# Optimization experiments

Hardware: AMD Instinct MI355X
Metric: run time of the kernel (lower is better)

The kernel has to match this reference:

```python
import jax, jax.numpy as jnp
import numpy as np

B, L, S = 4, 512, 100
NG, GS = 19, 5          # 19 clades of 5 species; species 95..99 are singleton clades
VOCAB = 6
HID = 512
HPOOL = 4               # num_attention_heads // 2
D = 64                  # hidden_size / num_attention_heads
ALL = HPOOL * D         # 256
FIRE_H = 32
TIME_SCALE = 1.0        # from time_enc = 'fire_1'
MAX_DIST = 20.0         # config.max_evol_dist


def setup_inputs() -> dict:
    key = jax.random.key(0)
    ks = jax.random.split(key, 10)
    return {
        "source_ids": jax.random.randint(ks[0], (B, L, S), 0, VOCAB, dtype=jnp.int32),
        "in_clade_phylo_dist": jax.random.uniform(ks[1], (S,), dtype=jnp.float32) * MAX_DIST,
        "attn_w_emb": jax.random.normal(ks[2], (VOCAB, HPOOL), dtype=jnp.float32) * 0.02,
        "value_emb": jax.random.normal(ks[3], (VOCAB, ALL), dtype=jnp.float32) * 0.02,
        "ffn_w": jax.random.normal(ks[4], (ALL, HID), dtype=jnp.float32) * 0.02,
        "ffn_b": jnp.zeros((HID,), dtype=jnp.float32),
        "embed_tab": jax.random.normal(ks[5], (VOCAB, HID), dtype=jnp.float32) * 0.02,
        "fire_c": jnp.float32(100.0),
        "fire_w1": jax.random.normal(ks[6], (FIRE_H,), dtype=jnp.float32) * 0.5,
        "fire_w2": jax.random.normal(ks[7], (FIRE_H,), dtype=jnp.float32) * 0.5,
    }


def reference(source_ids, in_clade_phylo_dist, attn_w_emb, value_emb,
              ffn_w, ffn_b, embed_tab, fire_c, fire_w1, fire_w2):
    # --- FIRE time bias: scalar MLP per species distance -> bias[s] ---
    c = jnp.maximum(fire_c, 0.0)
    rel = in_clade_phylo_dist * TIME_SCALE                      # [S]
    rel = jnp.log(c * rel + 1.0) / jnp.log(c * MAX_DIST + 1.0)  # [S]
    h = jax.nn.silu(rel[:, None] * fire_w1[None, :])            # [S, FIRE_H]
    bias = h @ fire_w2                                          # [S]

    # --- multi-species clades: embedding-based attention pooling ---
    grp = jnp.arange(NG * GS).reshape(NG, GS)                   # static clade layout
    ids_g = source_ids[..., :NG * GS].reshape(B, L, NG, GS)     # [B,L,NG,GS]
    scores = jnp.swapaxes(attn_w_emb[ids_g], -1, -2)            # [B,L,NG,H,GS]
    scores = scores + bias[grp][None, None, :, None, :]
    probs = jax.nn.softmax(scores, axis=-1)                     # dropout p=0 (eval)
    vals = value_emb[ids_g].reshape(B, L, NG, GS, HPOOL, D)     # [B,L,NG,GS,H,D]
    pooled = jnp.einsum('blnhg,blnghd->blnhd', probs, vals)     # [B,L,NG,H,D]
    pooled = pooled.reshape(B, L, NG, ALL)
    pooled = pooled @ ffn_w + ffn_b                             # [B,L,NG,HID]

    # --- singleton clades: plain embedding lookup ---
    singles = embed_tab[source_ids[..., NG * GS:]]              # [B,L,5,HID]

    return jnp.concatenate([pooled, singles], axis=-2)          # [B,L,24,HID]
```

## Files before the change

kernel.cpp:

```cpp
#include <hip/hip_runtime.h>

#define B_      4
#define L_      512
#define S_      100
#define NG_     19
#define GS_     5
#define VOCAB_  6
#define HID_    512
#define HPOOL_  4
#define D_      64
#define ALL_    256
#define FIREH_  32
#define MAXDIST_ 20.0f

typedef float f32x2 __attribute__((ext_vector_type(2)));
typedef float f32x4 __attribute__((ext_vector_type(4)));

#define NROWS_  (B_ * L_)

__global__ __launch_bounds__(128) void prep_kernel(
    const float* __restrict__ dist,
    const float* __restrict__ value_emb,
    const float* __restrict__ ffn_w,
    const float* __restrict__ fire_c,
    const float* __restrict__ fire_w1,
    const float* __restrict__ fire_w2,
    float* __restrict__ bias_out,
    float* __restrict__ W2_out)
{
  const int b = blockIdx.x;
  const int t = threadIdx.x;
  if (b < VOCAB_ * HPOOL_ * 4) {
    const int q   = b >> 2;
    const int col = (b & 3) * 128 + t;
    const int v = q >> 2, h = q & 3;
    float acc = 0.f;
#pragma unroll
    for (int k = 0; k < D_; ++k)
      acc = fmaf(value_emb[v * ALL_ + h * D_ + k],
                 ffn_w[(h * D_ + k) * HID_ + col], acc);
    W2_out[q * HID_ + col] = acc;
  } else if (t < S_) {
    const float c = fmaxf(fire_c[0], 0.f);
    const float denom = logf(fmaf(c, MAXDIST_, 1.f));
    const float rel = logf(fmaf(c, dist[t], 1.f)) / denom;
    float acc = 0.f;
#pragma unroll
    for (int i = 0; i < FIREH_; ++i) {
      const float x = rel * fire_w1[i];
      acc = fmaf(x / (1.f + __expf(-x)), fire_w2[i], acc);
    }
    bias_out[t] = acc;
  }
}

static __device__ __forceinline__ f32x4 fm4(float s, f32x4 w, f32x4 a) {
  a.x = fmaf(s, w.x, a.x);
  a.y = fmaf(s, w.y, a.y);
  a.z = fmaf(s, w.z, a.z);
  a.w = fmaf(s, w.w, a.w);
  return a;
}

__global__ __launch_bounds__(512, 4) void main_kernel(
    const int*   __restrict__ ids,
    const float* __restrict__ attn_w,
    const float* __restrict__ embed_tab,
    const float* __restrict__ ffn_b,
    const float* __restrict__ bias,
    const float* __restrict__ W2,
    float* __restrict__ out)
{
  const int blk = blockIdx.x;
  const int t   = threadIdx.x;
  const int bl0 = blk * 4;

  __shared__ int   s_ids[4 * S_];
  __shared__ float s_bias[S_];
  __shared__ float s_aw[VOCAB_ * HPOOL_];
  __shared__ __align__(16) float s_cw[4][NG_][24];

  if (t < 4 * S_) s_ids[t] = ids[bl0 * S_ + t];
  if (t >= 400 && t < 500) s_bias[t - 400] = bias[t - 400];
  if (t >= 488) s_aw[t - 488] = attn_w[t - 488];

  const int r  = t >> 7;
  const int c4 = (t & 127) * 4;
  f32x4 w2r[24];
#pragma unroll
  for (int q = 0; q < 24; ++q)
    w2r[q] = *(const f32x4*)&W2[q * HID_ + c4];
  const f32x4 bb = *(const f32x4*)&ffn_b[c4];

#pragma unroll
  for (int i = t; i < 4 * NG_ * 24; i += 512) ((float*)s_cw)[i] = 0.f;
  __syncthreads();

  if (t < 4 * NG_ * HPOOL_) {
    const int pr = t / 76;
    const int u  = t - pr * 76;
    const int n  = u >> 2, h = u & 3;
    int idg[GS_]; float p[GS_]; float m = -1e30f;
#pragma unroll
    for (int g = 0; g < GS_; ++g) {
      idg[g] = s_ids[pr * S_ + n * GS_ + g];
      p[g] = s_aw[idg[g] * HPOOL_ + h] + s_bias[n * GS_ + g];
      m = fmaxf(m, p[g]);
    }
    float s = 0.f;
#pragma unroll
    for (int g = 0; g < GS_; ++g) { p[g] = __expf(p[g] - m); s += p[g]; }
    const float inv = 1.f / s;
#pragma unroll
    for (int g = 0; g < GS_; ++g)
      s_cw[pr][n][idg[g] * HPOOL_ + h] += p[g] * inv;
  }
  __syncthreads();

  float* op = out + (size_t)(bl0 + r) * 24 * HID_ + c4;

#pragma unroll
  for (int j = 0; j < 5; ++j) {
    const int id = s_ids[r * S_ + NG_ * GS_ + j];
    *(f32x4*)(op + (NG_ + j) * HID_) =
        *(const f32x4*)&embed_tab[id * HID_ + c4];
  }

  for (int n = 0; n < NG_; ++n) {
    const f32x4* cw4 = (const f32x4*)s_cw[r][n];
    f32x4 acc = bb;
#pragma unroll
    for (int k = 0; k < 6; ++k) {
      const f32x4 c = cw4[k];
      acc = fm4(c.x, w2r[k * 4 + 0], acc);
      acc = fm4(c.y, w2r[k * 4 + 1], acc);
      acc = fm4(c.z, w2r[k * 4 + 2], acc);
      acc = fm4(c.w, w2r[k * 4 + 3], acc);
    }
    *(f32x4*)(op + n * HID_) = acc;
  }
}

extern "C" void kernel_launch(void* const* d_in, const int* in_sizes, int n_in,
                              void* d_out, int out_size, void* d_ws, size_t ws_size,
                              hipStream_t stream) {
  const int*   src_ids = (const int*)  d_in[0];
  const float* dist    = (const float*)d_in[1];
  const float* attn_w  = (const float*)d_in[2];
  const float* valemb  = (const float*)d_in[3];
  const float* ffn_w   = (const float*)d_in[4];
  const float* ffn_b   = (const float*)d_in[5];
  const float* emb_tab = (const float*)d_in[6];
  const float* fire_c  = (const float*)d_in[7];
  const float* fire_w1 = (const float*)d_in[8];
  const float* fire_w2 = (const float*)d_in[9];

  float* out  = (float*)d_out;
  float* ws   = (float*)d_ws;
  float* bias = ws;
  float* W2   = ws + 128;

  hipLaunchKernelGGL(prep_kernel, dim3(97), dim3(128), 0, stream,
                     dist, valemb, ffn_w, fire_c, fire_w1, fire_w2, bias, W2);
  hipLaunchKernelGGL(main_kernel, dim3(NROWS_ / 4), dim3(512), 0, stream,
                     src_ids, attn_w, emb_tab, ffn_b, bias, W2, out);
}
```

Baseline: 32.27 us.

## Fuse prep into main kernel, recomputing folded weights per block in shared memory

Removes the separate prep launch. Every block now recomputes the FIRE bias and the folded value_emb×ffn_w table (24×512) into shared memory, then pools 8 rows per 1024-thread block using 2-wide column vectors. This drops one kernel launch and the global round trip for the intermediate tables. The cost is redundant work in each of 256 blocks (each reads all of ffn_w, 512KB, and does about 400K FMAs) plus 48KB+ of shared memory per block, which limits occupancy.

```diff
diff --git a/kernel.cpp b/kernel.cpp
--- a/kernel.cpp
+++ b/kernel.cpp
@@ -17,86 +17,73 @@
 typedef float f32x4 __attribute__((ext_vector_type(4)));
 
 #define NROWS_  (B_ * L_)
+#define RPB_    8
+#define NBLK_   (NROWS_ / RPB_)
 
-__global__ __launch_bounds__(128) void prep_kernel(
+__global__ __launch_bounds__(1024) void fused_kernel(
+    const int*   __restrict__ ids,
     const float* __restrict__ dist,
+    const float* __restrict__ attn_w,
     const float* __restrict__ value_emb,
     const float* __restrict__ ffn_w,
+    const float* __restrict__ ffn_b,
+    const float* __restrict__ embed_tab,
     const float* __restrict__ fire_c,
     const float* __restrict__ fire_w1,
     const float* __restrict__ fire_w2,
-    float* __restrict__ bias_out,
-    float* __restrict__ W2_out)
+    float* __restrict__ out)
 {
-  const int b = blockIdx.x;
-  const int t = threadIdx.x;
-  if (b < VOCAB_ * HPOOL_ * 4) {
-    const int q   = b >> 2;
-    const int col = (b & 3) * 128 + t;
-    const int v = q >> 2, h = q & 3;
-    float acc = 0.f;
-#pragma unroll
-    for (int k = 0; k < D_; ++k)
-      acc = fmaf(value_emb[v * ALL_ + h * D_ + k],
-                 ffn_w[(h * D_ + k) * HID_ + col], acc);
-    W2_out[q * HID_ + col] = acc;
-  } else if (t < S_) {
+  const int blk  = blockIdx.x;
+  const int t    = threadIdx.x;
+  const int row0 = blk * RPB_;
+
+  __shared__ float s_W2[24 * HID_];
+  __shared__ __align__(16) float s_cw[RPB_][NG_][24];
+  __shared__ int   s_ids[RPB_ * S_];
+  __shared__ float s_bias[S_];
+  __shared__ float s_aw[VOCAB_ * HPOOL_];
+
+  if (t < RPB_ * S_) s_ids[t] = ids[row0 * S_ + t];
+  if (t >= 800 && t < 900) {
+    const int s = t - 800;
     const float c = fmaxf(fire_c[0], 0.f);
     const float denom = logf(fmaf(c, MAXDIST_, 1.f));
-    const float rel = logf(fmaf(c, dist[t], 1.f)) / denom;
+    const float rel = logf(fmaf(c, dist[s], 1.f)) / denom;
     float acc = 0.f;
 #pragma unroll
     for (int i = 0; i < FIREH_; ++i) {
       const float x = rel * fire_w1[i];
       acc = fmaf(x / (1.f + __expf(-x)), fire_w2[i], acc);
     }
-    bias_out[t] = acc;
+    s_bias[s] = acc;
   }
-}
+  if (t >= 1000) s_aw[t - 1000] = attn_w[t - 1000];
+#pragma unroll
+  for (int i = t; i < RPB_ * NG_ * 24; i += 1024) ((float*)s_cw)[i] = 0.f;
 
-static __device__ __forceinline__ f32x4 fm4(float s, f32x4 w, f32x4 a) {
-  a.x = fmaf(s, w.x, a.x);
-  a.y = fmaf(s, w.y, a.y);
-  a.z = fmaf(s, w.z, a.z);
-  a.w = fmaf(s, w.w, a.w);
-  return a;
-}
-
-__global__ __launch_bounds__(512, 4) void main_kernel(
-    const int*   __restrict__ ids,
-    const float* __restrict__ attn_w,
-    const float* __restrict__ embed_tab,
-    const float* __restrict__ ffn_b,
-    const float* __restrict__ bias,
-    const float* __restrict__ W2,
-    float* __restrict__ out)
-{
-  const int blk = blockIdx.x;
-  const int t   = threadIdx.x;
-  const int bl0 = blk * 4;
-
-  __shared__ int   s_ids[4 * S_];
-  __shared__ float s_bias[S_];
-  __shared__ float s_aw[VOCAB_ * HPOOL_];
-  __shared__ __align__(16) float s_cw[4][NG_][24];
-
-  if (t < 4 * S_) s_ids[t] = ids[bl0 * S_ + t];
-  if (t >= 400 && t < 500) s_bias[t - 400] = bias[t - 400];
-  if (t >= 488) s_aw[t - 488] = attn_w[t - 488];
-
-  const int r  = t >> 7;
-  const int c4 = (t & 127) * 4;
-  f32x4 w2r[24];
+  {
+    const int c    = t & 511;
+    const int half = t >> 9;
+    float wacc[12];
 #pragma unroll
-  for (int q = 0; q < 24; ++q)
-    w2r[q] = *(const f32x4*)&W2[q * HID_ + c4];
-  const f32x4 bb = *(const f32x4*)&ffn_b[c4];
-
+    for (int j = 0; j < 12; ++j) wacc[j] = 0.f;
 #pragma unroll
-  for (int i = t; i < 4 * NG_ * 24; i += 512) ((float*)s_cw)[i] = 0.f;
+    for (int h = 0; h < HPOOL_; ++h) {
+#pragma unroll 16
+      for (int k = 0; k < D_; ++k) {
+        const float f = ffn_w[(h * D_ + k) * HID_ + c];
+        wacc[0 * 4 + h] = fmaf(value_emb[(half * 3 + 0) * ALL_ + h * D_ + k], f, wacc[0 * 4 + h]);
+        wacc[1 * 4 + h] = fmaf(value_emb[(half * 3 + 1) * ALL_ + h * D_ + k], f, wacc[1 * 4 + h]);
+        wacc[2 * 4 + h] = fmaf(value_emb[(half * 3 + 2) * ALL_ + h * D_ + k], f, wacc[2 * 4 + h]);
+      }
+    }
+#pragma unroll
+    for (int j = 0; j < 12; ++j)
+      s_W2[(half * 12 + j) * HID_ + c] = wacc[j];
+  }
   __syncthreads();
 
-  if (t < 4 * NG_ * HPOOL_) {
+  if (t < RPB_ * NG_ * HPOOL_) {
     const int pr = t / 76;
     const int u  = t - pr * 76;
     const int n  = u >> 2, h = u & 3;
@@ -115,29 +102,45 @@
     for (int g = 0; g < GS_; ++g)
       s_cw[pr][n][idg[g] * HPOOL_ + h] += p[g] * inv;
   }
+
+  const int rr = t >> 8;
+  const int c2 = (t & 255) * 2;
+  f32x2 w2r[24];
+#pragma unroll
+  for (int q = 0; q < 24; ++q)
+    w2r[q] = *(const f32x2*)&s_W2[q * HID_ + c2];
+  const f32x2 bb = *(const f32x2*)&ffn_b[c2];
   __syncthreads();
 
-  float* op = out + (size_t)(bl0 + r) * 24 * HID_ + c4;
+#pragma unroll
+  for (int it = 0; it < 2; ++it) {
+    const int lr = it * 4 + rr;
+    float* op = out + (size_t)(row0 + lr) * 24 * HID_ + c2;
 
 #pragma unroll
-  for (int j = 0; j < 5; ++j) {
-    const int id = s_ids[r * S_ + NG_ * GS_ + j];
-    *(f32x4*)(op + (NG_ + j) * HID_) =
-        *(const f32x4*)&embed_tab[id * HID_ + c4];
-  }
+    for (int j = 0; j < 5; ++j) {
+      const int id = s_ids[lr * S_ + NG_ * GS_ + j];
+      *(f32x2*)(op + (NG_ + j) * HID_) =
+          *(const f32x2*)&embed_tab[id * HID_ + c2];
+    }
 
-  for (int n = 0; n < NG_; ++n) {
-    const f32x4* cw4 = (const f32x4*)s_cw[r][n];
-    f32x4 acc = bb;
+    for (int n = 0; n < NG_; ++n) {
+      const f32x4* cw4 = (const f32x4*)s_cw[lr][n];
+      f32x2 acc = bb;
 #pragma unroll
-    for (int k = 0; k < 6; ++k) {
-      const f32x4 c = cw4[k];
-      acc = fm4(c.x, w2r[k * 4 + 0], acc);
-      acc = fm4(c.y, w2r[k * 4 + 1], acc);
-      acc = fm4(c.z, w2r[k * 4 + 2], acc);
-      acc = fm4(c.w, w2r[k * 4 + 3], acc);
+      for (int k = 0; k < 6; ++k) {
+        const f32x4 c = cw4[k];
+        acc.x = fmaf(c.x, w2r[k * 4 + 0].x, acc.x);
+        acc.y = fmaf(c.x, w2r[k * 4 + 0].y, acc.y);
+        acc.x = fmaf(c.y, w2r[k * 4 + 1].x, acc.x);
+        acc.y = fmaf(c.y, w2r[k * 4 + 1].y, acc.y);
+        acc.x = fmaf(c.z, w2r[k * 4 + 2].x, acc.x);
+        acc.y = fmaf(c.z, w2r[k * 4 + 2].y, acc.y);
+        acc.x = fmaf(c.w, w2r[k * 4 + 3].x, acc.x);
+        acc.y = fmaf(c.w, w2r[k * 4 + 3].y, acc.y);
+      }
+      *(f32x2*)(op + n * HID_) = acc;
     }
-    *(f32x4*)(op + n * HID_) = acc;
   }
 }
 
@@ -155,13 +158,9 @@
   const float* fire_w1 = (const float*)d_in[8];
   const float* fire_w2 = (const float*)d_in[9];
 
-  float* out  = (float*)d_out;
-  float* ws   = (float*)d_ws;
-  float* bias = ws;
-  float* W2   = ws + 128;
+  float* out = (float*)d_out;
 
-  hipLaunchKernelGGL(prep_kernel, dim3(97), dim3(128), 0, stream,
-                     dist, valemb, ffn_w, fire_c, fire_w1, fire_w2, bias, W2);
-  hipLaunchKernelGGL(main_kernel, dim3(NROWS_ / 4), dim3(512), 0, stream,
-                     src_ids, attn_w, emb_tab, ffn_b, bias, W2, out);
+  hipLaunchKernelGGL(fused_kernel, dim3(NBLK_), dim3(1024), 0, stream,
+                     src_ids, dist, attn_w, valemb, ffn_w, ffn_b, emb_tab,
+                     fire_c, fire_w1, fire_w2, out);
 }
```

New measurement: 64.33 us. 99.3% more time.
